# Kernel optimization log

Measured on AMD Instinct MI355X. Metric: run time of the kernel, lower is better.

The kernel has to match this reference:

```python
import jax, jax.numpy as jnp
import numpy as np

B, T, D, H = 2, 2048, 1024, 8
HD = D // H

def setup_inputs() -> dict:
    key = jax.random.key(0)
    ks = jax.random.split(key, 6)
    s = 1.0 / np.sqrt(D)
    x = jax.random.normal(ks[0], (B, T, D), dtype=jnp.float32)
    Wq = jax.random.normal(ks[1], (D, D), dtype=jnp.float32) * s
    Wk = jax.random.normal(ks[2], (D, D), dtype=jnp.float32) * s
    Wv = jax.random.normal(ks[3], (D, D), dtype=jnp.float32) * s
    Wo = jax.random.normal(ks[4], (D, D), dtype=jnp.float32) * s
    bo = jnp.zeros((D,), dtype=jnp.float32)
    # theta[i] = 1 / 10000**(2i/H) as in _init_parameters
    theta = (1.0 / (10000.0 ** (2.0 * jnp.arange(H, dtype=jnp.float32) / H))).astype(jnp.float32)
    gamma = jnp.ones((D,), dtype=jnp.float32)   # group_norm weight
    beta = jnp.zeros((D,), dtype=jnp.float32)   # group_norm bias
    return {"x": x, "Wq": Wq, "Wk": Wk, "Wv": Wv, "Wo": Wo, "bo": bo,
            "theta": theta, "gamma": gamma, "beta": beta}

def reference(x, Wq, Wk, Wv, Wo, bo, theta, gamma, beta):
    b, t, d = x.shape
    h = theta.shape[0]
    hd = d // h
    q = (x @ Wq).reshape(b, t, h, hd)
    k = (x @ Wk).reshape(b, t, h, hd)
    v = (x @ Wv).reshape(b, t, h, hd)

    # decay mask: vectorized closed form of the O(T^2) python loop.
    # mask[i,j] = mean_h exp(-theta_h * (i-j)) for j<=i else 0
    pos = jnp.arange(t, dtype=jnp.float32)
    n = pos[:, None] - pos[None, :]                       # (T,T) i-j
    nn = jnp.maximum(n, 0.0)
    decay_mask = jnp.where(n >= 0,
                           jnp.mean(jnp.exp(-theta[None, None, :] * nn[:, :, None]), axis=-1),
                           0.0)                            # (T,T)

    scores = jnp.einsum('bthd,bshd->bths', q, k) / np.sqrt(hd)   # (B,T,H,T)
    scores = scores * decay_mask[None, :, None, :]
    causal = (n >= 0)[None, :, None, :]
    scores = jnp.where(causal, scores, -jnp.inf)
    retention = jax.nn.softmax(scores, axis=-1)
    out = jnp.einsum('bths,bshd->bthd', retention, v)            # (B,T,H,HD)

    # GroupNorm(num_heads, d_model): normalize each head's hd-chunk per token
    mu = out.mean(axis=-1, keepdims=True)
    var = out.var(axis=-1, keepdims=True)
    out = (out - mu) / jnp.sqrt(var + 1e-5)
    out = out.reshape(b, t, d) * gamma + beta

    return out @ Wo + bo
```

## Files before the change

kernel.cpp:

```cpp
#include <hip/hip_runtime.h>

#define B_SZ  2
#define T_SEQ 2048
#define D_MOD 1024
#define NH    8
#define HD    128

typedef __attribute__((ext_vector_type(8))) short short8;
typedef __attribute__((ext_vector_type(4))) float f32x4;

__device__ __forceinline__ short f2bf(float f) {
  unsigned u = __float_as_uint(f);
  unsigned r = u + 0x7fffu + ((u >> 16) & 1u);
  return (short)(r >> 16);
}

__device__ __forceinline__ void gld_lds16(const short* g, short* l) {
  __builtin_amdgcn_global_load_lds(
      (const __attribute__((address_space(1))) void*)g,
      (__attribute__((address_space(3))) void*)l, 16, 0, 0);
}

__global__ void decay_kernel(const float* __restrict__ theta,
                             float* __restrict__ dm) {
  int n = blockIdx.x * 256 + threadIdx.x;
  if (n >= T_SEQ) return;
  float nf = (float)n;
  float s = 0.f;
#pragma unroll
  for (int h = 0; h < NH; h++) s += __expf(-theta[h] * nf);
  dm[n] = s * (0.08838834764831845f / 8.0f);
}

__global__ __launch_bounds__(256) void cvt_x(const float* __restrict__ x,
                                             short* __restrict__ xb) {
  int i = (blockIdx.x * 256 + threadIdx.x) * 8;
  float4 a = *(const float4*)(x + i);
  float4 b = *(const float4*)(x + i + 4);
  short8 o;
  o[0] = f2bf(a.x); o[1] = f2bf(a.y); o[2] = f2bf(a.z); o[3] = f2bf(a.w);
  o[4] = f2bf(b.x); o[5] = f2bf(b.y); o[6] = f2bf(b.z); o[7] = f2bf(b.w);
  *(short8*)(xb + i) = o;
}

__global__ __launch_bounds__(256) void cvt_w(const float* __restrict__ Wq,
                                             const float* __restrict__ Wk,
                                             const float* __restrict__ Wv,
                                             const float* __restrict__ Wo,
                                             short* __restrict__ wt) {
  __shared__ float t[32][33];
  const int z = blockIdx.z;
  const float* __restrict__ W = (z == 0) ? Wq : (z == 1) ? Wk : (z == 2) ? Wv : Wo;
  short* __restrict__ dst = wt + (size_t)z * D_MOD * D_MOD;
  const int k0 = blockIdx.x * 32, n0 = blockIdx.y * 32;
  const int tx = threadIdx.x & 31, ty = threadIdx.x >> 5;
#pragma unroll
  for (int i = 0; i < 4; i++)
    t[ty * 4 + i][tx] = W[(size_t)(k0 + ty * 4 + i) * D_MOD + n0 + tx];
  __syncthreads();
#pragma unroll
  for (int i = 0; i < 4; i++)
    dst[(size_t)(n0 + ty * 4 + i) * D_MOD + k0 + tx] = f2bf(t[tx][ty * 4 + i]);
}

__global__ __launch_bounds__(256, 3) void gemm_qkv(
    const short* __restrict__ xb, const short* __restrict__ wt,
    short* __restrict__ qb, short* __restrict__ kb, short* __restrict__ vb) {
  __shared__ __align__(16) short As[128 * 32];
  __shared__ __align__(16) short Bs[128 * 32];
  const int tid = threadIdx.x;
  const int l = tid & 63, w = tid >> 6;
  const int wr = w >> 1, wc = w & 1;
  const int row0 = blockIdx.x * 128;
  const int h = blockIdx.y;
  const int col0 = h * 128;
  const short* __restrict__ Wt = wt + (size_t)blockIdx.z * D_MOD * D_MOD;
  short* __restrict__ dst = (blockIdx.z == 0) ? qb : (blockIdx.z == 1) ? kb : vb;

  f32x4 acc[4][4];
#pragma unroll
  for (int m = 0; m < 4; m++)
#pragma unroll
    for (int n = 0; n < 4; n++) acc[m][n] = (f32x4){0.f, 0.f, 0.f, 0.f};

  const int cA = w * 2;
  const int sr = l >> 2;
  const int skq = (l & 3) << 3;

#pragma unroll
  for (int i = 0; i < 2; i++) {
    int c = cA + i;
    gld_lds16(xb + (size_t)(row0 + c * 16 + sr) * D_MOD + skq, As + c * 512);
    gld_lds16(Wt + (size_t)(col0 + c * 16 + sr) * D_MOD + skq, Bs + c * 512);
  }
  for (int ks = 0; ks < 32; ks++) {
    __syncthreads();
    short8 af[4], bf[4];
#pragma unroll
    for (int m = 0; m < 4; m++)
      af[m] = *(const short8*)&As[(wr * 64 + m * 16 + (l & 15)) * 32 + (l >> 4) * 8];
#pragma unroll
    for (int n = 0; n < 4; n++)
      bf[n] = *(const short8*)&Bs[(wc * 64 + n * 16 + (l & 15)) * 32 + (l >> 4) * 8];
#pragma unroll
    for (int m = 0; m < 4; m++)
#pragma unroll
      for (int n = 0; n < 4; n++)
        acc[m][n] =
            __builtin_amdgcn_mfma_f32_16x16x32_bf16(af[m], bf[n], acc[m][n], 0, 0, 0);
    __syncthreads();
    if (ks < 31) {
      const int k0 = (ks + 1) * 32;
#pragma unroll
      for (int i = 0; i < 2; i++) {
        int c = cA + i;
        gld_lds16(xb + (size_t)(row0 + c * 16 + sr) * D_MOD + k0 + skq, As + c * 512);
        gld_lds16(Wt + (size_t)(col0 + c * 16 + sr) * D_MOD + k0 + skq, Bs + c * 512);
      }
    }
  }
#pragma unroll
  for (int m = 0; m < 4; m++) {
#pragma unroll
    for (int j = 0; j < 4; j++) {
      int row = row0 + wr * 64 + m * 16 + (l >> 4) * 4 + j;
      int bb = row >> 11, t = row & (T_SEQ - 1);
      size_t base = ((size_t)(bb * NH + h) * T_SEQ + t) * HD + wc * 64 + (l & 15);
#pragma unroll
      for (int n = 0; n < 4; n++) dst[base + n * 16] = f2bf(acc[m][n][j]);
    }
  }
}

__global__ __launch_bounds__(256, 3) void gemm_out(
    const short* __restrict__ yb, const short* __restrict__ wot,
    const float* __restrict__ bias, float* __restrict__ out) {
  __shared__ __align__(16) short As[128 * 32];
  __shared__ __align__(16) short Bs[128 * 32];
  const int tid = threadIdx.x;
  const int l = tid & 63, w = tid >> 6;
  const int wr = w >> 1, wc = w & 1;
  const int row0 = blockIdx.x * 128;
  const int col0 = blockIdx.y * 128;

  f32x4 acc[4][4];
#pragma unroll
  for (int m = 0; m < 4; m++)
#pragma unroll
    for (int n = 0; n < 4; n++) acc[m][n] = (f32x4){0.f, 0.f, 0.f, 0.f};

  const int cA = w * 2;
  const int sr = l >> 2;
  const int skq = (l & 3) << 3;

#pragma unroll
  for (int i = 0; i < 2; i++) {
    int c = cA + i;
    gld_lds16(yb + (size_t)(row0 + c * 16 + sr) * D_MOD + skq, As + c * 512);
    gld_lds16(wot + (size_t)(col0 + c * 16 + sr) * D_MOD + skq, Bs + c * 512);
  }
  for (int ks = 0; ks < 32; ks++) {
    __syncthreads();
    short8 af[4], bf[4];
#pragma unroll
    for (int m = 0; m < 4; m++)
      af[m] = *(const short8*)&As[(wr * 64 + m * 16 + (l & 15)) * 32 + (l >> 4) * 8];
#pragma unroll
    for (int n = 0; n < 4; n++)
      bf[n] = *(const short8*)&Bs[(wc * 64 + n * 16 + (l & 15)) * 32 + (l >> 4) * 8];
#pragma unroll
    for (int m = 0; m < 4; m++)
#pragma unroll
      for (int n = 0; n < 4; n++)
        acc[m][n] =
            __builtin_amdgcn_mfma_f32_16x16x32_bf16(af[m], bf[n], acc[m][n], 0, 0, 0);
    __syncthreads();
    if (ks < 31) {
      const int k0 = (ks + 1) * 32;
#pragma unroll
      for (int i = 0; i < 2; i++) {
        int c = cA + i;
        gld_lds16(yb + (size_t)(row0 + c * 16 + sr) * D_MOD + k0 + skq, As + c * 512);
        gld_lds16(wot + (size_t)(col0 + c * 16 + sr) * D_MOD + k0 + skq, Bs + c * 512);
      }
    }
  }
#pragma unroll
  for (int m = 0; m < 4; m++) {
#pragma unroll
    for (int j = 0; j < 4; j++) {
      int row = row0 + wr * 64 + m * 16 + (l >> 4) * 4 + j;
#pragma unroll
      for (int n = 0; n < 4; n++) {
        int col = col0 + wc * 64 + n * 16 + (l & 15);
        out[(size_t)row * D_MOD + col] = acc[m][n][j] + bias[col];
      }
    }
  }
}

__global__ __launch_bounds__(256, 2) void attn_kernel(
    const short* __restrict__ qg, const short* __restrict__ kg,
    const short* __restrict__ vg, const float* __restrict__ dm_g,
    const float* __restrict__ gamma, const float* __restrict__ beta,
    short* __restrict__ yb) {
  __shared__ __align__(16) short KT[2][8192];
  __shared__ __align__(16) short VT[2][8192];
  __shared__ __align__(16) short P2s[4][1024];
  __shared__ float dm_s[T_SEQ];

  const int tid = threadIdx.x;
  const int l = tid & 63, w = tid >> 6;
  const int lm = l & 15, lq = l >> 4;

  int qt = blockIdx.x & 31;
  const int h = (blockIdx.x >> 5) & 7;
  const int b = blockIdx.x >> 8;
  if (b) qt = 31 - qt;

  const size_t hoff = (size_t)(b * NH + h) * T_SEQ * HD;
  const short* __restrict__ Qh = qg + hoff;
  const short* __restrict__ Kh = kg + hoff;
  const short* __restrict__ Vh = vg + hoff;

  for (int i = tid * 4; i < T_SEQ; i += 1024)
    *(float4*)&dm_s[i] = *(const float4*)&dm_g[i];

  short8 qf[4];
  {
    int row = qt * 64 + w * 16 + lm;
#pragma unroll
    for (int kc = 0; kc < 4; kc++)
      qf[kc] = *(const short8*)(Qh + (size_t)row * HD + kc * 32 + lq * 8);
  }

  f32x4 zero4 = {0.f, 0.f, 0.f, 0.f};
  f32x4 o[8];
#pragma unroll
  for (int cb = 0; cb < 8; cb++) o[cb] = zero4;
  float m_r[4], l_r[4];
#pragma unroll
  for (int r = 0; r < 4; r++) { m_r[r] = -1e30f; l_r[r] = 0.f; }

  const int i_row0 = qt * 64 + w * 16 + lq * 4;
  const int d0 = l * 2;
  unsigned vv[16];

  {
    const int jP = qt * 64;
#pragma unroll
    for (int kc = 0; kc < 4; kc++)
      gld_lds16(Kh + (size_t)(jP + w * 16 + lm) * HD + kc * 32 + lq * 8,
                &KT[0][(w * 4 + kc) * 512]);
#pragma unroll
    for (int p = 0; p < 2; p++)
#pragma unroll
      for (int jj = 0; jj < 8; jj++)
        vv[p * 8 + jj] =
            *(const unsigned*)(Vh + (size_t)(jP + (w + p * 4) * 8 + jj) * HD + d0);
#pragma unroll
    for (int p = 0; p < 2; p++) {
      const int jl = (w + p * 4) * 8;
      const int kc2 = jl >> 5, bq = (jl >> 3) & 3;
#pragma unroll
      for (int dd = 0; dd < 2; dd++) {
        const int d = d0 + dd;
        short8 col;
#pragma unroll
        for (int jj = 0; jj < 8; jj++) {
          unsigned u = vv[p * 8 + jj];
          col[jj] = (short)(dd ? (u >> 16) : (u & 0xffffu));
        }
        *(short8*)&VT[0][(((d >> 4) * 2 + kc2) * 64 + bq * 16 + (d & 15)) * 8] = col;
      }
    }
  }
  __syncthreads();

  int cur = 0;
  for (int t = qt; t >= 0; --t) {
    const int j0 = t * 64;
    const int nxt = cur ^ 1;
    const bool pf = (t > 0);

    if (pf) {
      const int jn = j0 - 64;
#pragma unroll
      for (int kc = 0; kc < 4; kc++)
        gld_lds16(Kh + (size_t)(jn + w * 16 + lm) * HD + kc * 32 + lq * 8,
                  &KT[nxt][(w * 4 + kc) * 512]);
#pragma unroll
      for (int p = 0; p < 2; p++)
#pragma unroll
        for (int jj = 0; jj < 8; jj++)
          vv[p * 8 + jj] =
              *(const unsigned*)(Vh + (size_t)(jn + (w + p * 4) * 8 + jj) * HD + d0);
    }

    float s[4][4];
    __builtin_amdgcn_s_setprio(1);
#pragma unroll
    for (int jb = 0; jb < 4; jb++) {
      f32x4 acc = zero4;
#pragma unroll
      for (int kc = 0; kc < 4; kc++) {
        short8 kf = *(const short8*)&KT[cur][((jb * 4 + kc) * 64 + l) * 8];
        acc = __builtin_amdgcn_mfma_f32_16x16x32_bf16(qf[kc], kf, acc, 0, 0, 0);
      }
      const int j = j0 + jb * 16 + lm;
#pragma unroll
      for (int r = 0; r < 4; r++) {
        int delta = (i_row0 + r) - j;
        float sv = acc[r] * dm_s[delta & (T_SEQ - 1)];
        s[jb][r] = (delta >= 0) ? sv : -__builtin_inff();
      }
    }
    __builtin_amdgcn_s_setprio(0);

    float smax[4];
#pragma unroll
    for (int r = 0; r < 4; r++)
      smax[r] = fmaxf(fmaxf(s[0][r], s[1][r]), fmaxf(s[2][r], s[3][r]));
    int grow = 0;
#pragma unroll
    for (int r = 0; r < 4; r++) grow |= (smax[r] > m_r[r] + 4.0f) ? 1 : 0;
    if (__any(grow)) {
#pragma unroll
      for (int r = 0; r < 4; r++) {
        float mx = smax[r];
        mx = fmaxf(mx, __shfl_xor(mx, 1));
        mx = fmaxf(mx, __shfl_xor(mx, 2));
        mx = fmaxf(mx, __shfl_xor(mx, 4));
        mx = fmaxf(mx, __shfl_xor(mx, 8));
        float mnew = fmaxf(m_r[r], mx);
        float fac = __expf(m_r[r] - mnew);
        m_r[r] = mnew;
        l_r[r] *= fac;
#pragma unroll
        for (int cb = 0; cb < 8; cb++) o[cb][r] *= fac;
      }
    }

    float lsum[4] = {0.f, 0.f, 0.f, 0.f};
#pragma unroll
    for (int jb = 0; jb < 4; jb++) {
      const int jl2 = jb * 16 + lm;
      const int pbase = (jl2 >> 5) * 512 + ((jl2 & 31) >> 3) * 128 + (jl2 & 7);
#pragma unroll
      for (int r = 0; r < 4; r++) {
        float pv = __expf(s[jb][r] - m_r[r]);
        lsum[r] += pv;
        P2s[w][pbase + (lq * 4 + r) * 8] = f2bf(pv);
      }
    }
#pragma unroll
    for (int r = 0; r < 4; r++) {
      float sm = lsum[r];
      sm += __shfl_xor(sm, 1); sm += __shfl_xor(sm, 2);
      sm += __shfl_xor(sm, 4); sm += __shfl_xor(sm, 8);
      l_r[r] += sm;
    }

    __builtin_amdgcn_s_setprio(1);
#pragma unroll
    for (int kc2 = 0; kc2 < 2; kc2++) {
      short8 pb = *(const short8*)&P2s[w][kc2 * 512 + l * 8];
#pragma unroll
      for (int cb = 0; cb < 8; cb++) {
        short8 vf = *(const short8*)&VT[cur][((cb * 2 + kc2) * 64 + l) * 8];
        o[cb] = __builtin_amdgcn_mfma_f32_16x16x32_bf16(pb, vf, o[cb], 0, 0, 0);
      }
    }
    __builtin_amdgcn_s_setprio(0);

    if (pf) {
#pragma unroll
      for (int p = 0; p < 2; p++) {
        const int jl = (w + p * 4) * 8;
        const int kc2 = jl >> 5, bq = (jl >> 3) & 3;
#pragma unroll
        for (int dd = 0; dd < 2; dd++) {
          const int d = d0 + dd;
          short8 col;
#pragma unroll
          for (int jj = 0; jj < 8; jj++) {
            unsigned u = vv[p * 8 + jj];
            col[jj] = (short)(dd ? (u >> 16) : (u & 0xffffu));
          }
          *(short8*)&VT[nxt][(((d >> 4) * 2 + kc2) * 64 + bq * 16 + (d & 15)) * 8] =
              col;
        }
      }
    }
    __syncthreads();
    cur = nxt;
  }

  float mu[4], rstd[4];
#pragma unroll
  for (int r = 0; r < 4; r++) {
    float inv = 1.0f / l_r[r];
    float sum = 0.f, sq = 0.f;
#pragma unroll
    for (int cb = 0; cb < 8; cb++) {
      float v2 = o[cb][r] * inv;
      o[cb][r] = v2;
      sum += v2;
      sq += v2 * v2;
    }
    sum += __shfl_xor(sum, 1); sum += __shfl_xor(sum, 2);
    sum += __shfl_xor(sum, 4); sum += __shfl_xor(sum, 8);
    sq += __shfl_xor(sq, 1); sq += __shfl_xor(sq, 2);
    sq += __shfl_xor(sq, 4); sq += __shfl_xor(sq, 8);
    float m2 = sum * (1.f / 128.f);
    mu[r] = m2;
    rstd[r] = rsqrtf(sq * (1.f / 128.f) - m2 * m2 + 1e-5f);
  }
  const int trow = qt * 64 + w * 16 + lq * 4;
#pragma unroll
  for (int cb = 0; cb < 8; cb++) {
    const int dcol = h * HD + cb * 16 + lm;
    const float g = gamma[dcol], be = beta[dcol];
#pragma unroll
    for (int r = 0; r < 4; r++) {
      float val = (o[cb][r] - mu[r]) * rstd[r] * g + be;
      yb[(size_t)(b * T_SEQ + trow + r) * D_MOD + dcol] = f2bf(val);
    }
  }
}

extern "C" void kernel_launch(void* const* d_in, const int* in_sizes, int n_in,
                              void* d_out, int out_size, void* d_ws,
                              size_t ws_size, hipStream_t stream) {
  const float* x     = (const float*)d_in[0];
  const float* Wq    = (const float*)d_in[1];
  const float* Wk    = (const float*)d_in[2];
  const float* Wv    = (const float*)d_in[3];
  const float* Wo    = (const float*)d_in[4];
  const float* bo    = (const float*)d_in[5];
  const float* theta = (const float*)d_in[6];
  const float* gamma = (const float*)d_in[7];
  const float* beta  = (const float*)d_in[8];
  float* out = (float*)d_out;

  char* ws = (char*)d_ws;
  const size_t MB = 1024 * 1024;
  short* qb = (short*)(ws + 0 * MB);
  short* kb = (short*)(ws + 8 * MB);
  short* vb = (short*)(ws + 16 * MB);
  short* yb = (short*)(ws + 24 * MB);
  short* xb = (short*)(ws + 32 * MB);
  short* wt = (short*)(ws + 40 * MB);
  float* dm = (float*)(ws + 48 * MB);

  decay_kernel<<<dim3(8), dim3(256), 0, stream>>>(theta, dm);
  cvt_x<<<dim3(2048), dim3(256), 0, stream>>>(x, xb);
  cvt_w<<<dim3(32, 32, 4), dim3(256), 0, stream>>>(Wq, Wk, Wv, Wo, wt);
  gemm_qkv<<<dim3(32, 8, 3), dim3(256), 0, stream>>>(xb, wt, qb, kb, vb);
  attn_kernel<<<dim3(512), dim3(256), 0, stream>>>(qb, kb, vb, dm, gamma, beta, yb);
  gemm_out<<<dim3(32, 8), dim3(256), 0, stream>>>(
      yb, wt + (size_t)3 * D_MOD * D_MOD, bo, out);
}
```

Before: 225.4 us.

## Compute transposed QK scores and pass P via shuffles instead of LDS

Swaps the MFMA operand order so each lane holds scores for a single query row, which turns the softmax max and sum reductions into two cross-lane shuffles and keeps the running max and sum as scalars per lane. The probabilities are packed to bf16 with v_cvt_pk_bf16_f32 and moved into the PV operand layout through lane shuffles, removing the P2s shared-memory round trip and the per-element stores. The block index is also remapped so that consecutive physical blocks spread across heads and batches instead of taking the reversed query-tile order for the second batch. The cost is extra shuffle and select instructions per tile, which may cost more than the LDS traffic they replace.

```diff
diff --git a/kernel.cpp b/kernel.cpp
--- a/kernel.cpp
+++ b/kernel.cpp
@@ -206,17 +206,17 @@
     short* __restrict__ yb) {
   __shared__ __align__(16) short KT[2][8192];
   __shared__ __align__(16) short VT[2][8192];
-  __shared__ __align__(16) short P2s[4][1024];
   __shared__ float dm_s[T_SEQ];
 
   const int tid = threadIdx.x;
   const int l = tid & 63, w = tid >> 6;
   const int lm = l & 15, lq = l >> 4;
 
-  int qt = blockIdx.x & 31;
-  const int h = (blockIdx.x >> 5) & 7;
-  const int b = blockIdx.x >> 8;
-  if (b) qt = 31 - qt;
+  const unsigned pbid = blockIdx.x;
+  const unsigned lbid = (pbid & 7) * 64 + (pbid >> 3);
+  const int qt = lbid & 31;
+  const int h = (lbid >> 5) & 7;
+  const int b = lbid >> 8;
 
   const size_t hoff = (size_t)(b * NH + h) * T_SEQ * HD;
   const short* __restrict__ Qh = qg + hoff;
@@ -238,12 +238,12 @@
   f32x4 o[8];
 #pragma unroll
   for (int cb = 0; cb < 8; cb++) o[cb] = zero4;
-  float m_r[4], l_r[4];
-#pragma unroll
-  for (int r = 0; r < 4; r++) { m_r[r] = -1e30f; l_r[r] = 0.f; }
-
-  const int i_row0 = qt * 64 + w * 16 + lq * 4;
+  float m_r = -1e30f, l_r = 0.f;
+
+  const int i_row = qt * 64 + w * 16 + lm;
   const int d0 = l * 2;
+  const int srcA = lm + 32 * (lq & 1);
+  const int srcB = srcA + 16;
   unsigned vv[16];
 
   {
@@ -305,66 +305,82 @@
 #pragma unroll
       for (int kc = 0; kc < 4; kc++) {
         short8 kf = *(const short8*)&KT[cur][((jb * 4 + kc) * 64 + l) * 8];
-        acc = __builtin_amdgcn_mfma_f32_16x16x32_bf16(qf[kc], kf, acc, 0, 0, 0);
-      }
-      const int j = j0 + jb * 16 + lm;
+        acc = __builtin_amdgcn_mfma_f32_16x16x32_bf16(kf, qf[kc], acc, 0, 0, 0);
+      }
 #pragma unroll
       for (int r = 0; r < 4; r++) {
-        int delta = (i_row0 + r) - j;
+        int delta = i_row - (j0 + jb * 16 + lq * 4 + r);
         float sv = acc[r] * dm_s[delta & (T_SEQ - 1)];
         s[jb][r] = (delta >= 0) ? sv : -__builtin_inff();
       }
     }
     __builtin_amdgcn_s_setprio(0);
 
-    float smax[4];
-#pragma unroll
-    for (int r = 0; r < 4; r++)
-      smax[r] = fmaxf(fmaxf(s[0][r], s[1][r]), fmaxf(s[2][r], s[3][r]));
-    int grow = 0;
-#pragma unroll
-    for (int r = 0; r < 4; r++) grow |= (smax[r] > m_r[r] + 4.0f) ? 1 : 0;
-    if (__any(grow)) {
+    float lmax = fmaxf(fmaxf(fmaxf(s[0][0], s[0][1]), fmaxf(s[0][2], s[0][3])),
+                       fmaxf(fmaxf(s[1][0], s[1][1]), fmaxf(s[1][2], s[1][3])));
+    lmax = fmaxf(lmax,
+                 fmaxf(fmaxf(fmaxf(s[2][0], s[2][1]), fmaxf(s[2][2], s[2][3])),
+                       fmaxf(fmaxf(s[3][0], s[3][1]), fmaxf(s[3][2], s[3][3]))));
+    if (__any(lmax > m_r + 4.0f)) {
+      float mx = lmax;
+      mx = fmaxf(mx, __shfl_xor(mx, 16));
+      mx = fmaxf(mx, __shfl_xor(mx, 32));
+      float mnew = fmaxf(m_r, mx);
+      float fac = __expf(m_r - mnew);
+      m_r = mnew;
+      l_r *= fac;
+      float facr[4];
+#pragma unroll
+      for (int r = 0; r < 4; r++) facr[r] = __shfl(fac, lq * 4 + r);
+#pragma unroll
+      for (int cb = 0; cb < 8; cb++)
+#pragma unroll
+        for (int r = 0; r < 4; r++) o[cb][r] *= facr[r];
+    }
+
+    float lsum = 0.f;
+#pragma unroll
+    for (int jb = 0; jb < 4; jb++)
 #pragma unroll
       for (int r = 0; r < 4; r++) {
-        float mx = smax[r];
-        mx = fmaxf(mx, __shfl_xor(mx, 1));
-        mx = fmaxf(mx, __shfl_xor(mx, 2));
-        mx = fmaxf(mx, __shfl_xor(mx, 4));
-        mx = fmaxf(mx, __shfl_xor(mx, 8));
-        float mnew = fmaxf(m_r[r], mx);
-        float fac = __expf(m_r[r] - mnew);
-        m_r[r] = mnew;
-        l_r[r] *= fac;
-#pragma unroll
-        for (int cb = 0; cb < 8; cb++) o[cb][r] *= fac;
-      }
-    }
-
-    float lsum[4] = {0.f, 0.f, 0.f, 0.f};
+        float pv = __expf(s[jb][r] - m_r);
+        s[jb][r] = pv;
+        lsum += pv;
+      }
+    lsum += __shfl_xor(lsum, 16);
+    lsum += __shfl_xor(lsum, 32);
+    l_r += lsum;
+
+    unsigned pw[4][2];
 #pragma unroll
     for (int jb = 0; jb < 4; jb++) {
-      const int jl2 = jb * 16 + lm;
-      const int pbase = (jl2 >> 5) * 512 + ((jl2 & 31) >> 3) * 128 + (jl2 & 7);
-#pragma unroll
-      for (int r = 0; r < 4; r++) {
-        float pv = __expf(s[jb][r] - m_r[r]);
-        lsum[r] += pv;
-        P2s[w][pbase + (lq * 4 + r) * 8] = f2bf(pv);
-      }
-    }
-#pragma unroll
-    for (int r = 0; r < 4; r++) {
-      float sm = lsum[r];
-      sm += __shfl_xor(sm, 1); sm += __shfl_xor(sm, 2);
-      sm += __shfl_xor(sm, 4); sm += __shfl_xor(sm, 8);
-      l_r[r] += sm;
+      asm("v_cvt_pk_bf16_f32 %0, %1, %2"
+          : "=v"(pw[jb][0]) : "v"(s[jb][0]), "v"(s[jb][1]));
+      asm("v_cvt_pk_bf16_f32 %0, %1, %2"
+          : "=v"(pw[jb][1]) : "v"(s[jb][2]), "v"(s[jb][3]));
     }
 
     __builtin_amdgcn_s_setprio(1);
 #pragma unroll
     for (int kc2 = 0; kc2 < 2; kc2++) {
-      short8 pb = *(const short8*)&P2s[w][kc2 * 512 + l * 8];
+      unsigned w0a = __shfl((int)pw[2 * kc2][0], srcA);
+      unsigned w0b = __shfl((int)pw[2 * kc2 + 1][0], srcA);
+      unsigned w1a = __shfl((int)pw[2 * kc2][1], srcA);
+      unsigned w1b = __shfl((int)pw[2 * kc2 + 1][1], srcA);
+      unsigned w2a = __shfl((int)pw[2 * kc2][0], srcB);
+      unsigned w2b = __shfl((int)pw[2 * kc2 + 1][0], srcB);
+      unsigned w3a = __shfl((int)pw[2 * kc2][1], srcB);
+      unsigned w3b = __shfl((int)pw[2 * kc2 + 1][1], srcB);
+      const bool hi = (lq & 2) != 0;
+      unsigned w0 = hi ? w0b : w0a;
+      unsigned w1 = hi ? w1b : w1a;
+      unsigned w2 = hi ? w2b : w2a;
+      unsigned w3 = hi ? w3b : w3a;
+      short8 pb;
+      pb[0] = (short)(w0 & 0xffffu); pb[1] = (short)(w0 >> 16);
+      pb[2] = (short)(w1 & 0xffffu); pb[3] = (short)(w1 >> 16);
+      pb[4] = (short)(w2 & 0xffffu); pb[5] = (short)(w2 >> 16);
+      pb[6] = (short)(w3 & 0xffffu); pb[7] = (short)(w3 >> 16);
 #pragma unroll
       for (int cb = 0; cb < 8; cb++) {
         short8 vf = *(const short8*)&VT[cur][((cb * 2 + kc2) * 64 + l) * 8];
@@ -396,14 +412,16 @@
     cur = nxt;
   }
 
+  float linv[4];
+#pragma unroll
+  for (int r = 0; r < 4; r++) linv[r] = 1.0f / __shfl(l_r, lq * 4 + r);
   float mu[4], rstd[4];
 #pragma unroll
   for (int r = 0; r < 4; r++) {
-    float inv = 1.0f / l_r[r];
     float sum = 0.f, sq = 0.f;
 #pragma unroll
     for (int cb = 0; cb < 8; cb++) {
-      float v2 = o[cb][r] * inv;
+      float v2 = o[cb][r] * linv[r];
       o[cb][r] = v2;
       sum += v2;
       sq += v2 * v2;
```

After: 219.4 us. 1.03x faster.
